# Kernel tuning notes

Measured on AMD Instinct MI355X. Metric: run time of the kernel, lower is better.

## Reference

```python
import jax, jax.numpy as jnp
import numpy as np

N, E = 20000, 320000
IN, H, C = 1024, 8, 64
HC = H * C
EDGE_DIM = 16
NUM_GRAPHS = 8
LEAKY_SLOPE = 0.2
LN_EPS = 1e-5


def setup_inputs() -> dict:
    key = jax.random.key(0)
    ks = jax.random.split(key, 12)
    s = 0.05
    return {
        "x": jax.random.normal(ks[0], (N, IN), jnp.float32),
        "edge_attr": jax.random.normal(ks[1], (E, EDGE_DIM), jnp.float32),
        "edge_index": jax.random.randint(ks[2], (2, E), 0, N, dtype=jnp.int64),
        "batch": jnp.sort(jax.random.randint(ks[3], (N,), 0, NUM_GRAPHS, dtype=jnp.int64)),
        "W_src": jax.random.normal(ks[4], (IN, HC), jnp.float32) * s,
        "W_dst": jax.random.normal(ks[5], (IN, HC), jnp.float32) * s,
        "att_src": jax.random.normal(ks[6], (H, C), jnp.float32) * s,
        "att_dst": jax.random.normal(ks[7], (H, C), jnp.float32) * s,
        "bias": jnp.zeros((HC,), jnp.float32),
        "ln_gamma": jnp.ones((HC,), jnp.float32),
        "ln_beta": jnp.zeros((HC,), jnp.float32),
        "prelu_a": jnp.full((HC,), 0.25, jnp.float32),
    }


def reference(x, edge_attr, edge_index, batch, W_src, W_dst, att_src, att_dst,
              bias, ln_gamma, ln_beta, prelu_a):
    # Eval mode: node/edge feature dropout and attention dropout are identity.
    # with_edge == 'N': edge_attr is unused by the conv.
    n = x.shape[0]
    src, dst = edge_index[0], edge_index[1]

    xs = (x @ W_src).reshape(n, H, C)   # source-side projections
    xd = (x @ W_dst).reshape(n, H, C)   # dest-side projections
    a_src = jnp.einsum('nhc,hc->nh', xs, att_src)
    a_dst = jnp.einsum('nhc,hc->nh', xd, att_dst)

    # edge scores + softmax over incoming edges of each destination node
    e = jax.nn.leaky_relu(a_src[src] + a_dst[dst], LEAKY_SLOPE)  # [E,H]
    m = jax.ops.segment_max(e, dst, num_segments=n)              # [N,H]
    m = jax.lax.stop_gradient(jnp.where(jnp.isfinite(m), m, 0.0))
    ex = jnp.exp(e - m[dst])
    denom = jax.ops.segment_sum(ex, dst, num_segments=n)
    alpha = ex / (denom[dst] + 1e-16)                            # [E,H]

    msg = alpha[:, :, None] * xs[src]                            # [E,H,C]
    out = jax.ops.segment_sum(msg, dst, num_segments=n).reshape(n, HC) + bias

    # norm_type == 'layer': the per-graph boolean-mask loop applies LayerNorm
    # row-wise; with sorted batch ids this equals a single LayerNorm over all
    # nodes (LayerNorm has no cross-row statistics).
    mu = jnp.mean(out, axis=-1, keepdims=True)
    var = jnp.mean(jnp.square(out - mu), axis=-1, keepdims=True)
    y = (out - mu) * jax.lax.rsqrt(var + LN_EPS) * ln_gamma + ln_beta

    # PReLU with per-channel slope
    return jnp.where(y >= 0, y, prelu_a * y)
```

## Files before the change

kernel.cpp:

```cpp
#include <hip/hip_runtime.h>
#include <hip/hip_bf16.h>

#define N_NODES 20000
#define N_EDGES 320000
#define IN_DIM  1024
#define H_HEADS 8
#define C_CH    64
#define HC      512
#define LEAKY   0.2f
#define LN_EPS  1e-5f

#define BCOLS 576
#define NCT   36
#define NKT   32
#define NRT   1250


typedef short bf16x8 __attribute__((ext_vector_type(8)));
typedef float f32x4  __attribute__((ext_vector_type(4)));

__device__ __forceinline__ unsigned short f2bf(float f) {
    union { float f; unsigned int u; } c; c.f = f;
    unsigned int u = c.u;
    unsigned int r = (u + 0x7fffu + ((u >> 16) & 1u)) >> 16;
    return (unsigned short)r;
}
__device__ __forceinline__ float bf2f(unsigned int h) {
    union { unsigned int u; float f; } c; c.u = h << 16; return c.f;
}
__device__ __forceinline__ unsigned int cvtpk(float lo, float hi) {
    unsigned int r;
    asm("v_cvt_pk_bf16_f32 %0, %1, %2" : "=v"(r) : "v"(lo), "v"(hi));
    return r;
}

#define DEG_BLOCKS 1250
#define CONV_BLOCKS NRT
#define PREP_BLOCKS NKT

__global__ __launch_bounds__(256) void fused_pre(
        const float* __restrict__ x,
        const int* __restrict__ ei,
        const float* __restrict__ Wsrc,
        const float* __restrict__ Wdst,
        const float* __restrict__ att_src,
        const float* __restrict__ att_dst,
        short* __restrict__ xbt,
        short* __restrict__ wbtt,
        int* __restrict__ deg) {
    __shared__ short sw[32 * 512];
    __shared__ float f1[32][8], f2[32][8];
    int t   = threadIdx.x;
    int bid = blockIdx.x;

    if (bid < DEG_BLOCKS) {
        int e = bid * 256 + t;
        atomicAdd(&deg[ei[N_EDGES + e]], 1);
        return;
    }

    if (bid < DEG_BLOCKS + CONV_BLOCKS) {
        int rt   = bid - DEG_BLOCKS;
        int lane = t & 63, w = t >> 6;
        int lr = lane & 15, lg = lane >> 4;
        const float* xr = x + (size_t)(rt * 16 + lr) * IN_DIM;
        #pragma unroll
        for (int i = 0; i < 8; ++i) {
            int kt = w + i * 4;
            float4 f = *(const float4*)(xr + kt * 32 + lg * 8);
            float4 g = *(const float4*)(xr + kt * 32 + lg * 8 + 4);
            uint4 r;
            r.x = cvtpk(f.x, f.y);  r.y = cvtpk(f.z, f.w);
            r.z = cvtpk(g.x, g.y);  r.w = cvtpk(g.z, g.w);
            *(uint4*)(xbt + (((size_t)rt * 32 + kt) << 9) + lane * 8) = r;
        }
        return;
    }

    int kt = bid - (DEG_BLOCKS + CONV_BLOCKS);
    int k0 = kt * 32;
    for (int i = t; i < 32 * 128; i += 256) {
        int kk = i >> 7, g4 = i & 127;
        float4 v = *(const float4*)(Wsrc + (size_t)(k0 + kk) * HC + g4 * 4);
        uint2 p;
        p.x = cvtpk(v.x, v.y);  p.y = cvtpk(v.z, v.w);
        *(uint2*)(&sw[kk * 512 + g4 * 4]) = p;
    }
    {
        int kk = t >> 3, h = t & 7;
        const float* wsr = Wsrc + (size_t)(k0 + kk) * HC + h * 64;
        const float* wdr = Wdst + (size_t)(k0 + kk) * HC + h * 64;
        const float* a1  = att_src + h * 64;
        const float* a2  = att_dst + h * 64;
        float s1 = 0.f, s2 = 0.f;
        #pragma unroll 8
        for (int c = 0; c < 64; ++c) {
            s1 += wsr[c] * a1[c];
            s2 += wdr[c] * a2[c];
        }
        f1[kk][h] = s1;  f2[kk][h] = s2;
    }
    __syncthreads();
    for (int idx = t; idx < NCT * 64; idx += 256) {
        int ct = idx >> 6, sl = idx & 63;
        int lr = sl & 15, lg = sl >> 4;
        int col = ct * 16 + lr;
        union { short v[8]; uint4 u; } pk;
        #pragma unroll
        for (int j = 0; j < 8; ++j) {
            int kk = lg * 8 + j;
            short val;
            if (col < 512)      val = sw[kk * 512 + col];
            else if (col < 520) val = (short)f2bf(f1[kk][col - 512]);
            else if (col < 528) val = (short)f2bf(f2[kk][col - 520]);
            else                val = 0;
            pk.v[j] = val;
        }
        *(uint4*)(wbtt + (((size_t)ct * 32 + kt) << 9) + sl * 8) = pk.u;
    }
}

#define NCOLT 6
#define NROWT 313
#define NWG (NROWT * NCOLT)

__global__ __launch_bounds__(256) void gemm_scan(
        const short* __restrict__ xbt,
        const short* __restrict__ wbtt,
        short* __restrict__ xsb,
        float* __restrict__ a_srcv,
        float* __restrict__ a_dstv,
        const int* __restrict__ deg,
        int* __restrict__ off,
        int* __restrict__ cursor) {
    int t = threadIdx.x;

    if (blockIdx.x == NWG) {
        __shared__ int wtot[2];
        int lane = t & 63, wv = t >> 6;
        const int4* deg4 = (const int4*)deg;
        int s = 0;
        if (t < 125) {
            #pragma unroll
            for (int j = 0; j < 40; ++j) {
                int4 u = deg4[t * 40 + j];
                s += u.x + u.y + u.z + u.w;
            }
        }
        int v = s;
        #pragma unroll
        for (int o = 1; o < 64; o <<= 1) {
            int u = __shfl_up(v, o);
            if (lane >= o) v += u;
        }
        if (lane == 63 && wv < 2) wtot[wv] = v;
        __syncthreads();
        int add = (wv == 1) ? wtot[0] : 0;
        int run = add + v - s;
        if (t < 125) {
            int4* off4 = (int4*)off;
            int4* cur4 = (int4*)cursor;
            #pragma unroll
            for (int j = 0; j < 40; ++j) {
                int4 u = deg4[t * 40 + j];
                int4 o_;
                o_.x = run;
                o_.y = o_.x + u.x;
                o_.z = o_.y + u.y;
                o_.w = o_.z + u.z;
                off4[t * 40 + j] = o_;
                cur4[t * 40 + j] = o_;
                run = o_.w + u.w;
            }
            if (t == 124) off[N_NODES] = run;
        }
        return;
    }

    int orig = blockIdx.x;
    const int q = NWG >> 3, r = NWG & 7;
    int xcd  = orig & 7;
    int wgid = (xcd < r ? xcd * (q + 1) : r * (q + 1) + (xcd - r) * q) + (orig >> 3);
    int colblk = wgid % NCOLT;
    int rowblk = wgid / NCOLT;
    int row0 = (rowblk < NROWT - 1) ? rowblk * 64 : (N_NODES - 64);

    int lane = t & 63;
    int w    = t >> 6;
    int lr   = lane & 15;
    int lg   = lane >> 4;
    int rtw  = (row0 >> 4) + (w >> 1) * 2;
    int ctw  = colblk * 6 + (w & 1) * 3;

    const short* pa0 = xbt  + (((size_t)(rtw + 0) * 32) << 9) + lane * 8;
    const short* pa1 = xbt  + (((size_t)(rtw + 1) * 32) << 9) + lane * 8;
    const short* pb0 = wbtt + (((size_t)(ctw + 0) * 32) << 9) + lane * 8;
    const short* pb1 = wbtt + (((size_t)(ctw + 1) * 32) << 9) + lane * 8;
    const short* pb2 = wbtt + (((size_t)(ctw + 2) * 32) << 9) + lane * 8;

    f32x4 acc[2][3] = {};

    #pragma unroll 4
    for (int kt = 0; kt < NKT; ++kt) {
        bf16x8 a0 = *(const bf16x8*)(pa0 + kt * 512);
        bf16x8 a1 = *(const bf16x8*)(pa1 + kt * 512);
        bf16x8 b0 = *(const bf16x8*)(pb0 + kt * 512);
        bf16x8 b1 = *(const bf16x8*)(pb1 + kt * 512);
        bf16x8 b2 = *(const bf16x8*)(pb2 + kt * 512);
        acc[0][0] = __builtin_amdgcn_mfma_f32_16x16x32_bf16(a0, b0, acc[0][0], 0, 0, 0);
        acc[0][1] = __builtin_amdgcn_mfma_f32_16x16x32_bf16(a0, b1, acc[0][1], 0, 0, 0);
        acc[0][2] = __builtin_amdgcn_mfma_f32_16x16x32_bf16(a0, b2, acc[0][2], 0, 0, 0);
        acc[1][0] = __builtin_amdgcn_mfma_f32_16x16x32_bf16(a1, b0, acc[1][0], 0, 0, 0);
        acc[1][1] = __builtin_amdgcn_mfma_f32_16x16x32_bf16(a1, b1, acc[1][1], 0, 0, 0);
        acc[1][2] = __builtin_amdgcn_mfma_f32_16x16x32_bf16(a1, b2, acc[1][2], 0, 0, 0);
    }

    #pragma unroll
    for (int mi = 0; mi < 2; ++mi) {
        #pragma unroll
        for (int rr = 0; rr < 4; ++rr) {
            int row = (rtw + mi) * 16 + lg * 4 + rr;
            #pragma unroll
            for (int ni = 0; ni < 3; ++ni) {
                int col = (ctw + ni) * 16 + lr;
                float v = acc[mi][ni][rr];
                if (col < 512)      xsb[(size_t)row * HC + col] = (short)f2bf(v);
                else if (col < 520) a_srcv[(size_t)row * 8 + (col - 512)] = v;
                else if (col < 528) a_dstv[(size_t)row * 8 + (col - 520)] = v;
            }
        }
    }
}

__global__ __launch_bounds__(256) void edge_scatter(
        const int* __restrict__ ei,
        int* __restrict__ cursor,
        int* __restrict__ csr_src) {
    int e = blockIdx.x * 256 + threadIdx.x;
    int d = ei[N_EDGES + e];
    int idx = atomicAdd(&cursor[d], 1);
    csr_src[idx] = ei[e];
}

__global__ __launch_bounds__(256) void aggregate_ln(
        const int* __restrict__ off,
        const int* __restrict__ csr_src,
        const float* __restrict__ a_srcv,
        const float* __restrict__ a_dstv,
        const short* __restrict__ xsb,
        const float* __restrict__ bias,
        const float* __restrict__ gamma,
        const float* __restrict__ beta,
        const float* __restrict__ prelu_a,
        float* __restrict__ out) {
    int lane = threadIdx.x & 63;
    int n    = blockIdx.x * 4 + (threadIdx.x >> 6);
    int ch0  = lane * 8;
    int h    = lane >> 3;

    int start = off[n], end = off[n + 1];
    float ad  = a_dstv[(size_t)n * 8 + h];

    float acc[8] = {};
    float wsum = 0.f;

    int i = start;
    for (; i + 1 < end; i += 2) {
        int s0 = __builtin_amdgcn_readfirstlane(csr_src[i]);
        int s1 = __builtin_amdgcn_readfirstlane(csr_src[i + 1]);
        float sc0 = a_srcv[(size_t)s0 * 8 + h] + ad;
        float sc1 = a_srcv[(size_t)s1 * 8 + h] + ad;
        uint4 u0 = *(const uint4*)(xsb + (size_t)s0 * HC + ch0);
        uint4 u1 = *(const uint4*)(xsb + (size_t)s1 * HC + ch0);
        sc0 = (sc0 >= 0.f) ? sc0 : LEAKY * sc0;
        sc1 = (sc1 >= 0.f) ? sc1 : LEAKY * sc1;
        float w0 = __expf(sc0);
        float w1 = __expf(sc1);
        acc[0] = fmaf(w0, bf2f(u0.x & 0xffffu), acc[0]);
        acc[1] = fmaf(w0, bf2f(u0.x >> 16),     acc[1]);
        acc[2] = fmaf(w0, bf2f(u0.y & 0xffffu), acc[2]);
        acc[3] = fmaf(w0, bf2f(u0.y >> 16),     acc[3]);
        acc[4] = fmaf(w0, bf2f(u0.z & 0xffffu), acc[4]);
        acc[5] = fmaf(w0, bf2f(u0.z >> 16),     acc[5]);
        acc[6] = fmaf(w0, bf2f(u0.w & 0xffffu), acc[6]);
        acc[7] = fmaf(w0, bf2f(u0.w >> 16),     acc[7]);
        acc[0] = fmaf(w1, bf2f(u1.x & 0xffffu), acc[0]);
        acc[1] = fmaf(w1, bf2f(u1.x >> 16),     acc[1]);
        acc[2] = fmaf(w1, bf2f(u1.y & 0xffffu), acc[2]);
        acc[3] = fmaf(w1, bf2f(u1.y >> 16),     acc[3]);
        acc[4] = fmaf(w1, bf2f(u1.z & 0xffffu), acc[4]);
        acc[5] = fmaf(w1, bf2f(u1.z >> 16),     acc[5]);
        acc[6] = fmaf(w1, bf2f(u1.w & 0xffffu), acc[6]);
        acc[7] = fmaf(w1, bf2f(u1.w >> 16),     acc[7]);
        wsum += w0 + w1;
    }
    if (i < end) {
        int s0 = __builtin_amdgcn_readfirstlane(csr_src[i]);
        float sc0 = a_srcv[(size_t)s0 * 8 + h] + ad;
        uint4 u0 = *(const uint4*)(xsb + (size_t)s0 * HC + ch0);
        sc0 = (sc0 >= 0.f) ? sc0 : LEAKY * sc0;
        float w0 = __expf(sc0);
        acc[0] = fmaf(w0, bf2f(u0.x & 0xffffu), acc[0]);
        acc[1] = fmaf(w0, bf2f(u0.x >> 16),     acc[1]);
        acc[2] = fmaf(w0, bf2f(u0.y & 0xffffu), acc[2]);
        acc[3] = fmaf(w0, bf2f(u0.y >> 16),     acc[3]);
        acc[4] = fmaf(w0, bf2f(u0.z & 0xffffu), acc[4]);
        acc[5] = fmaf(w0, bf2f(u0.z >> 16),     acc[5]);
        acc[6] = fmaf(w0, bf2f(u0.w & 0xffffu), acc[6]);
        acc[7] = fmaf(w0, bf2f(u0.w >> 16),     acc[7]);
        wsum += w0;
    }

    float inv = 1.f / (wsum + 1e-16f);
    float4 b0 = *(const float4*)(bias + ch0);
    float4 b1 = *(const float4*)(bias + ch0 + 4);
    float v8[8];
    float psum = 0.f, psq = 0.f;
    const float bb[8] = {b0.x, b0.y, b0.z, b0.w, b1.x, b1.y, b1.z, b1.w};
    #pragma unroll
    for (int j = 0; j < 8; ++j) {
        v8[j] = acc[j] * inv + bb[j];
        psum += v8[j];
        psq  += v8[j] * v8[j];
    }
    #pragma unroll
    for (int o = 32; o > 0; o >>= 1) {
        psum += __shfl_xor(psum, o);
        psq  += __shfl_xor(psq, o);
    }
    float mu   = psum * (1.f / (float)HC);
    float var  = psq * (1.f / (float)HC) - mu * mu;
    float rstd = rsqrtf(var + LN_EPS);

    float4 g0 = *(const float4*)(gamma + ch0);
    float4 g1 = *(const float4*)(gamma + ch0 + 4);
    float4 e0 = *(const float4*)(beta + ch0);
    float4 e1 = *(const float4*)(beta + ch0 + 4);
    float4 p0 = *(const float4*)(prelu_a + ch0);
    float4 p1 = *(const float4*)(prelu_a + ch0 + 4);
    const float gg[8] = {g0.x, g0.y, g0.z, g0.w, g1.x, g1.y, g1.z, g1.w};
    const float ee[8] = {e0.x, e0.y, e0.z, e0.w, e1.x, e1.y, e1.z, e1.w};
    const float pp[8] = {p0.x, p0.y, p0.z, p0.w, p1.x, p1.y, p1.z, p1.w};
    float y[8];
    #pragma unroll
    for (int j = 0; j < 8; ++j) {
        float v = (v8[j] - mu) * rstd * gg[j] + ee[j];
        y[j] = (v >= 0.f) ? v : pp[j] * v;
    }
    float4* o4 = (float4*)(out + (size_t)n * HC + ch0);
    o4[0] = make_float4(y[0], y[1], y[2], y[3]);
    o4[1] = make_float4(y[4], y[5], y[6], y[7]);
}

extern "C" void kernel_launch(void* const* d_in, const int* in_sizes, int n_in,
                              void* d_out, int out_size, void* d_ws, size_t ws_size,
                              hipStream_t stream) {
    const float* x        = (const float*)d_in[0];
    const int*   ei       = (const int*)d_in[2];
    const float* Wsrc     = (const float*)d_in[4];
    const float* Wdst     = (const float*)d_in[5];
    const float* att_src  = (const float*)d_in[6];
    const float* att_dst  = (const float*)d_in[7];
    const float* bias     = (const float*)d_in[8];
    const float* gamma    = (const float*)d_in[9];
    const float* beta     = (const float*)d_in[10];
    const float* prelu_a  = (const float*)d_in[11];
    float* out            = (float*)d_out;

    char*  ws = (char*)d_ws;
    size_t o  = 0;
    auto alloc = [&](size_t bytes) -> void* {
        void* p = ws + o;
        o += (bytes + 255) & ~(size_t)255;
        return p;
    };
    short* wbtt    = (short*)alloc(sizeof(short) * NCT * NKT * 512);
    short* xsb     = (short*)alloc(sizeof(short) * (size_t)N_NODES * HC);
    float* a_srcv  = (float*)alloc(sizeof(float) * N_NODES * 8);
    float* a_dstv  = (float*)alloc(sizeof(float) * N_NODES * 8);
    int*   deg     = (int*)alloc(sizeof(int) * N_NODES);
    int*   off     = (int*)alloc(sizeof(int) * (N_NODES + 1));
    int*   cursor  = (int*)alloc(sizeof(int) * N_NODES);
    int*   csr_src = (int*)alloc(sizeof(int) * N_EDGES);

    short* xbt = (short*)d_out;

    hipMemsetAsync(deg, 0, sizeof(int) * N_NODES, stream);

    fused_pre<<<DEG_BLOCKS + CONV_BLOCKS + PREP_BLOCKS, 256, 0, stream>>>(
        x, ei, Wsrc, Wdst, att_src, att_dst, xbt, wbtt, deg);

    gemm_scan<<<NWG + 1, 256, 0, stream>>>(
        xbt, wbtt, xsb, a_srcv, a_dstv, deg, off, cursor);

    edge_scatter<<<N_EDGES / 256, 256, 0, stream>>>(ei, cursor, csr_src);

    aggregate_ln<<<N_NODES / 4, 256, 0, stream>>>(
        off, csr_src, a_srcv, a_dstv, xsb, bias, gamma, beta, prelu_a, out);
}
```

Measured before the change: 174.5 us.

## Fuse x bf16 conversion into GEMM via LDS panel and merge edge scatter

Removes the separate x-to-bf16 pre-conversion pass and its round trip through global memory. Each GEMM block now loads a 32-row fp32 slab of x, converts it into a swizzled LDS panel, and computes all 576 output columns with 9 column tiles per wave. The degree scan moves to its own single-block kernel, and the edge scatter is merged into the GEMM launch as extra blocks so the two overlap. In exchange there are fewer GEMM blocks with heavier per-block register and LDS use, plus one more tiny launch for the scan.

```diff
diff --git a/kernel.cpp b/kernel.cpp
--- a/kernel.cpp
+++ b/kernel.cpp
@@ -13,7 +13,6 @@
 #define BCOLS 576
 #define NCT   36
 #define NKT   32
-#define NRT   1250
 
 
 typedef short bf16x8 __attribute__((ext_vector_type(8)));
@@ -35,17 +34,14 @@
 }
 
 #define DEG_BLOCKS 1250
-#define CONV_BLOCKS NRT
 #define PREP_BLOCKS NKT
 
-__global__ __launch_bounds__(256) void fused_pre(
-        const float* __restrict__ x,
+__global__ __launch_bounds__(256) void pre_kernel(
         const int* __restrict__ ei,
         const float* __restrict__ Wsrc,
         const float* __restrict__ Wdst,
         const float* __restrict__ att_src,
         const float* __restrict__ att_dst,
-        short* __restrict__ xbt,
         short* __restrict__ wbtt,
         int* __restrict__ deg) {
     __shared__ short sw[32 * 512];
@@ -59,25 +55,7 @@
         return;
     }
 
-    if (bid < DEG_BLOCKS + CONV_BLOCKS) {
-        int rt   = bid - DEG_BLOCKS;
-        int lane = t & 63, w = t >> 6;
-        int lr = lane & 15, lg = lane >> 4;
-        const float* xr = x + (size_t)(rt * 16 + lr) * IN_DIM;
-        #pragma unroll
-        for (int i = 0; i < 8; ++i) {
-            int kt = w + i * 4;
-            float4 f = *(const float4*)(xr + kt * 32 + lg * 8);
-            float4 g = *(const float4*)(xr + kt * 32 + lg * 8 + 4);
-            uint4 r;
-            r.x = cvtpk(f.x, f.y);  r.y = cvtpk(f.z, f.w);
-            r.z = cvtpk(g.x, g.y);  r.w = cvtpk(g.z, g.w);
-            *(uint4*)(xbt + (((size_t)rt * 32 + kt) << 9) + lane * 8) = r;
-        }
-        return;
-    }
-
-    int kt = bid - (DEG_BLOCKS + CONV_BLOCKS);
+    int kt = bid - DEG_BLOCKS;
     int k0 = kt * 32;
     for (int i = t; i < 32 * 128; i += 256) {
         int kk = i >> 7, g4 = i & 127;
@@ -120,109 +98,128 @@
     }
 }
 
-#define NCOLT 6
-#define NROWT 313
-#define NWG (NROWT * NCOLT)
-
-__global__ __launch_bounds__(256) void gemm_scan(
-        const short* __restrict__ xbt,
+__global__ void scan_kernel(const int* __restrict__ deg,
+                            int* __restrict__ off,
+                            int* __restrict__ cursor) {
+    __shared__ int wtot[2];
+    int t = threadIdx.x;
+    int lane = t & 63, w = t >> 6;
+    const int4* deg4 = (const int4*)deg;
+    int s = 0;
+    if (t < 125) {
+        #pragma unroll
+        for (int j = 0; j < 40; ++j) {
+            int4 u = deg4[t * 40 + j];
+            s += u.x + u.y + u.z + u.w;
+        }
+    }
+    int v = s;
+    #pragma unroll
+    for (int o = 1; o < 64; o <<= 1) {
+        int u = __shfl_up(v, o);
+        if (lane >= o) v += u;
+    }
+    if (lane == 63) wtot[w] = v;
+    __syncthreads();
+    int add = (w == 1) ? wtot[0] : 0;
+    int run = add + v - s;
+    if (t < 125) {
+        int4* off4 = (int4*)off;
+        int4* cur4 = (int4*)cursor;
+        #pragma unroll
+        for (int j = 0; j < 40; ++j) {
+            int4 u = deg4[t * 40 + j];
+            int4 o_;
+            o_.x = run;
+            o_.y = o_.x + u.x;
+            o_.z = o_.y + u.y;
+            o_.w = o_.z + u.z;
+            off4[t * 40 + j] = o_;
+            cur4[t * 40 + j] = o_;
+            run = o_.w + u.w;
+        }
+        if (t == 124) off[N_NODES] = run;
+    }
+}
+
+#define GEMM_BLKS 625
+#define SCAT_BLKS 1250
+
+__global__ __launch_bounds__(256) void gemm_scatter(
+        const float* __restrict__ x,
         const short* __restrict__ wbtt,
         short* __restrict__ xsb,
         float* __restrict__ a_srcv,
         float* __restrict__ a_dstv,
-        const int* __restrict__ deg,
-        int* __restrict__ off,
-        int* __restrict__ cursor) {
+        const int* __restrict__ ei,
+        int* __restrict__ cursor,
+        int* __restrict__ csr_src) {
+    __shared__ short Apan[32 * 128 * 8];
     int t = threadIdx.x;
 
-    if (blockIdx.x == NWG) {
-        __shared__ int wtot[2];
-        int lane = t & 63, wv = t >> 6;
-        const int4* deg4 = (const int4*)deg;
-        int s = 0;
-        if (t < 125) {
-            #pragma unroll
-            for (int j = 0; j < 40; ++j) {
-                int4 u = deg4[t * 40 + j];
-                s += u.x + u.y + u.z + u.w;
-            }
-        }
-        int v = s;
-        #pragma unroll
-        for (int o = 1; o < 64; o <<= 1) {
-            int u = __shfl_up(v, o);
-            if (lane >= o) v += u;
-        }
-        if (lane == 63 && wv < 2) wtot[wv] = v;
-        __syncthreads();
-        int add = (wv == 1) ? wtot[0] : 0;
-        int run = add + v - s;
-        if (t < 125) {
-            int4* off4 = (int4*)off;
-            int4* cur4 = (int4*)cursor;
-            #pragma unroll
-            for (int j = 0; j < 40; ++j) {
-                int4 u = deg4[t * 40 + j];
-                int4 o_;
-                o_.x = run;
-                o_.y = o_.x + u.x;
-                o_.z = o_.y + u.y;
-                o_.w = o_.z + u.z;
-                off4[t * 40 + j] = o_;
-                cur4[t * 40 + j] = o_;
-                run = o_.w + u.w;
-            }
-            if (t == 124) off[N_NODES] = run;
-        }
+    if (blockIdx.x >= GEMM_BLKS) {
+        int e = (blockIdx.x - GEMM_BLKS) * 256 + t;
+        int d = ei[N_EDGES + e];
+        int idx = atomicAdd(&cursor[d], 1);
+        csr_src[idx] = ei[e];
         return;
     }
 
     int orig = blockIdx.x;
-    const int q = NWG >> 3, r = NWG & 7;
+    const int q = GEMM_BLKS >> 3, r = GEMM_BLKS & 7;
     int xcd  = orig & 7;
     int wgid = (xcd < r ? xcd * (q + 1) : r * (q + 1) + (xcd - r) * q) + (orig >> 3);
-    int colblk = wgid % NCOLT;
-    int rowblk = wgid / NCOLT;
-    int row0 = (rowblk < NROWT - 1) ? rowblk * 64 : (N_NODES - 64);
+    int row0 = wgid * 32;
 
     int lane = t & 63;
     int w    = t >> 6;
     int lr   = lane & 15;
     int lg   = lane >> 4;
-    int rtw  = (row0 >> 4) + (w >> 1) * 2;
-    int ctw  = colblk * 6 + (w & 1) * 3;
-
-    const short* pa0 = xbt  + (((size_t)(rtw + 0) * 32) << 9) + lane * 8;
-    const short* pa1 = xbt  + (((size_t)(rtw + 1) * 32) << 9) + lane * 8;
-    const short* pb0 = wbtt + (((size_t)(ctw + 0) * 32) << 9) + lane * 8;
-    const short* pb1 = wbtt + (((size_t)(ctw + 1) * 32) << 9) + lane * 8;
-    const short* pb2 = wbtt + (((size_t)(ctw + 2) * 32) << 9) + lane * 8;
-
-    f32x4 acc[2][3] = {};
-
-    #pragma unroll 4
+
+    #pragma unroll 8
+    for (int i = 0; i < 32; ++i) {
+        int v   = t + 256 * i;
+        int row = v >> 8;
+        int c   = v & 255;
+        float4 f = *(const float4*)(x + (size_t)(row0 + row) * IN_DIM + c * 4);
+        int slot = row * 128 + ((c >> 1) ^ (row & 7));
+        uint2 p;
+        p.x = cvtpk(f.x, f.y);  p.y = cvtpk(f.z, f.w);
+        *(uint2*)(&Apan[slot * 8 + (c & 1) * 4]) = p;
+    }
+    __syncthreads();
+
+    int ct0 = w * 9;
+    const short* pb[9];
+    #pragma unroll
+    for (int ni = 0; ni < 9; ++ni)
+        pb[ni] = wbtt + (((size_t)(ct0 + ni) * 32) << 9) + lane * 8;
+
+    f32x4 acc[2][9] = {};
+
+    #pragma unroll 2
     for (int kt = 0; kt < NKT; ++kt) {
-        bf16x8 a0 = *(const bf16x8*)(pa0 + kt * 512);
-        bf16x8 a1 = *(const bf16x8*)(pa1 + kt * 512);
-        bf16x8 b0 = *(const bf16x8*)(pb0 + kt * 512);
-        bf16x8 b1 = *(const bf16x8*)(pb1 + kt * 512);
-        bf16x8 b2 = *(const bf16x8*)(pb2 + kt * 512);
-        acc[0][0] = __builtin_amdgcn_mfma_f32_16x16x32_bf16(a0, b0, acc[0][0], 0, 0, 0);
-        acc[0][1] = __builtin_amdgcn_mfma_f32_16x16x32_bf16(a0, b1, acc[0][1], 0, 0, 0);
-        acc[0][2] = __builtin_amdgcn_mfma_f32_16x16x32_bf16(a0, b2, acc[0][2], 0, 0, 0);
-        acc[1][0] = __builtin_amdgcn_mfma_f32_16x16x32_bf16(a1, b0, acc[1][0], 0, 0, 0);
-        acc[1][1] = __builtin_amdgcn_mfma_f32_16x16x32_bf16(a1, b1, acc[1][1], 0, 0, 0);
-        acc[1][2] = __builtin_amdgcn_mfma_f32_16x16x32_bf16(a1, b2, acc[1][2], 0, 0, 0);
+        int kc  = kt * 4 + lg;
+        int sA0 = (lr      ) * 128 + (kc ^ (lr & 7));
+        int sA1 = (lr + 16 ) * 128 + (kc ^ (lr & 7));
+        bf16x8 a0 = *(const bf16x8*)(&Apan[sA0 * 8]);
+        bf16x8 a1 = *(const bf16x8*)(&Apan[sA1 * 8]);
+        #pragma unroll
+        for (int ni = 0; ni < 9; ++ni) {
+            bf16x8 b = *(const bf16x8*)(pb[ni] + kt * 512);
+            acc[0][ni] = __builtin_amdgcn_mfma_f32_16x16x32_bf16(a0, b, acc[0][ni], 0, 0, 0);
+            acc[1][ni] = __builtin_amdgcn_mfma_f32_16x16x32_bf16(a1, b, acc[1][ni], 0, 0, 0);
+        }
     }
 
     #pragma unroll
     for (int mi = 0; mi < 2; ++mi) {
         #pragma unroll
         for (int rr = 0; rr < 4; ++rr) {
-            int row = (rtw + mi) * 16 + lg * 4 + rr;
+            int row = row0 + mi * 16 + lg * 4 + rr;
             #pragma unroll
-            for (int ni = 0; ni < 3; ++ni) {
-                int col = (ctw + ni) * 16 + lr;
+            for (int ni = 0; ni < 9; ++ni) {
+                int col = (ct0 + ni) * 16 + lr;
                 float v = acc[mi][ni][rr];
                 if (col < 512)      xsb[(size_t)row * HC + col] = (short)f2bf(v);
                 else if (col < 520) a_srcv[(size_t)row * 8 + (col - 512)] = v;
@@ -230,16 +227,6 @@
             }
         }
     }
-}
-
-__global__ __launch_bounds__(256) void edge_scatter(
-        const int* __restrict__ ei,
-        int* __restrict__ cursor,
-        int* __restrict__ csr_src) {
-    int e = blockIdx.x * 256 + threadIdx.x;
-    int d = ei[N_EDGES + e];
-    int idx = atomicAdd(&cursor[d], 1);
-    csr_src[idx] = ei[e];
 }
 
 __global__ __launch_bounds__(256) void aggregate_ln(
@@ -383,17 +370,15 @@
     int*   cursor  = (int*)alloc(sizeof(int) * N_NODES);
     int*   csr_src = (int*)alloc(sizeof(int) * N_EDGES);
 
-    short* xbt = (short*)d_out;
-
     hipMemsetAsync(deg, 0, sizeof(int) * N_NODES, stream);
 
-    fused_pre<<<DEG_BLOCKS + CONV_BLOCKS + PREP_BLOCKS, 256, 0, stream>>>(
-        x, ei, Wsrc, Wdst, att_src, att_dst, xbt, wbtt, deg);
-
-    gemm_scan<<<NWG + 1, 256, 0, stream>>>(
-        xbt, wbtt, xsb, a_srcv, a_dstv, deg, off, cursor);
-
-    edge_scatter<<<N_EDGES / 256, 256, 0, stream>>>(ei, cursor, csr_src);
+    pre_kernel<<<DEG_BLOCKS + PREP_BLOCKS, 256, 0, stream>>>(
+        ei, Wsrc, Wdst, att_src, att_dst, wbtt, deg);
+
+    scan_kernel<<<1, 128, 0, stream>>>(deg, off, cursor);
+
+    gemm_scatter<<<GEMM_BLKS + SCAT_BLKS, 256, 0, stream>>>(
+        x, wbtt, xsb, a_srcv, a_dstv, ei, cursor, csr_src);
 
     aggregate_ln<<<N_NODES / 4, 256, 0, stream>>>(
         off, csr_src, a_srcv, a_dstv, xsb, bias, gamma, beta, prelu_a, out);
```

Measured after the change: 199.1 us. +14.1%, slower.
